# Optimization experiments

Measured on AMD Instinct MI355X. Metric: run time of the kernel, lower is better.

## Reference

```python
import jax, jax.numpy as jnp
import numpy as np

N = 50000
E = 800000
H = 8          # attention heads
C = 16         # per-head channels (128 // 8)
D = 128        # in_channels == num_hidden_channels
L = 2          # num_layers
NEG_SLOPE = 0.2
LN_EPS = 1e-12


def setup_inputs() -> dict:
    key = jax.random.key(0)
    ks = jax.random.split(key, 8)
    x = jax.random.normal(ks[0], (N, D), dtype=jnp.float32)
    edge_index = jax.random.randint(ks[1], (2, E), 0, N).astype(jnp.int64)
    W = jax.random.normal(ks[2], (L, D, D), dtype=jnp.float32) * 0.1
    att = jax.random.normal(ks[3], (L, H, C), dtype=jnp.float32) * 0.1
    bias = jnp.zeros((L, D), dtype=jnp.float32)
    out_W = jax.random.normal(ks[4], (D, D), dtype=jnp.float32) * 0.1
    out_b = jnp.zeros((D,), dtype=jnp.float32)
    ln_g = jnp.ones((D,), dtype=jnp.float32)
    ln_b = jnp.zeros((D,), dtype=jnp.float32)
    return {"x": x, "edge_index": edge_index, "W": W, "att": att, "bias": bias,
            "out_W": out_W, "out_b": out_b, "ln_g": ln_g, "ln_b": ln_b,
            "num_trg_nodes": 25000}


def gatv2_conv(x, src, dst, W_l, a_l, b_l):
    # share_weights=True: same linear map for source and target nodes
    h = (x @ W_l).reshape(N, H, C)               # [N,H,C]
    hs = h[src]                                  # [E,H,C] gather source
    hd = h[dst]                                  # [E,H,C] gather target
    e = jax.nn.leaky_relu(hs + hd, NEG_SLOPE)    # GATv2: LeakyReLU before attention vector
    logits = jnp.einsum('ehc,hc->eh', e, a_l)    # [E,H]
    # segment softmax over edges grouped by destination node
    seg_max = jax.ops.segment_max(logits, dst, num_segments=N)   # [N,H]
    ex = jnp.exp(logits - seg_max[dst])
    seg_sum = jax.ops.segment_sum(ex, dst, num_segments=N)       # [N,H]
    alpha = ex / (seg_sum[dst] + 1e-16)                          # [E,H]
    msg = (hs * alpha[..., None]).reshape(E, H * C)              # weighted messages
    out = jax.ops.segment_sum(msg, dst, num_segments=N)          # [N,H*C]
    return out + b_l


def reference(x, edge_index, W, att, bias, out_W, out_b, ln_g, ln_b, num_trg_nodes):
    src = edge_index[0]
    dst = edge_index[1]
    for i in range(L):
        x = gatv2_conv(x, src, dst, W[i], att[i], bias[i])
        if i != L - 1:
            # eval mode: dropout is identity; torch nn.GELU is exact erf gelu
            x = jax.nn.gelu(x, approximate=False)
    # output head: Linear -> LayerNorm(eps=1e-12) -> Dropout(identity in eval)
    y = x[:num_trg_nodes] @ out_W + out_b
    mu = jnp.mean(y, axis=-1, keepdims=True)
    var = jnp.mean(jnp.square(y - mu), axis=-1, keepdims=True)
    y = (y - mu) / jnp.sqrt(var + LN_EPS) * ln_g + ln_b
    return y
```

## Files before the change

### kernel.cpp

```cpp
#include <hip/hip_runtime.h>
#include <math.h>


#define D 128
#define H 8
#define C 16
#define NBIN 256

typedef __attribute__((ext_vector_type(8))) short bf16x8v;
typedef __attribute__((ext_vector_type(4))) float f32x4v;

static __device__ __forceinline__ float bf2f(unsigned int u16) {
    union { unsigned int i; float f; } x; x.i = u16 << 16; return x.f;
}
static __device__ __forceinline__ unsigned short f2bf(float f) {
    union { float f; unsigned int i; } x; x.f = f;
    unsigned int r = x.i + 0x7fffu + ((x.i >> 16) & 1u);
    return (unsigned short)(r >> 16);
}
static __device__ __forceinline__ float gelu_f(float v) {
    return 0.5f * v * (1.0f + erff(v * 0.70710678118654752f));
}
static __device__ __forceinline__ float exp2_hw(float x) {
    float r;
    asm("v_exp_f32 %0, %1" : "=v"(r) : "v"(x));
    return r;
}
#define DPP_ADD(v, ctrl) \
    (v) += __builtin_bit_cast(float, __builtin_amdgcn_update_dpp( \
        0, __builtin_bit_cast(int, (v)), (ctrl), 0xf, 0xf, true))

template<int IN_BF, int OUT_BF, int GELU>
static __device__ __forceinline__ void gemm_body(
    int bid, const void* __restrict__ Xv, const unsigned short* __restrict__ Wt,
    const float* __restrict__ bias, void* __restrict__ Outv, int nrows)
{
    const int t  = threadIdx.x;
    const int l  = t & 63;
    const int wv = t >> 6;
    const int g  = l >> 4;
    const int r  = l & 15;
    const int m0 = bid * 64;
    const int row = m0 + wv * 16 + r;
    const bool rv = row < nrows;
    const uint4* Wt4 = reinterpret_cast<const uint4*>(Wt);

    bf16x8v afrag[4];
#pragma unroll
    for (int kk = 0; kk < 4; ++kk) {
        int kg = kk * 4 + g;
        float v[8];
        if (IN_BF) {
            uint4 q = make_uint4(0, 0, 0, 0);
            if (rv) q = reinterpret_cast<const uint4*>(Xv)[(size_t)row * 16 + kg];
            if (GELU) {
                unsigned int qq[4] = {q.x, q.y, q.z, q.w};
#pragma unroll
                for (int j = 0; j < 4; ++j) {
                    v[2 * j]     = gelu_f(bf2f(qq[j] & 0xffffu));
                    v[2 * j + 1] = gelu_f(bf2f(qq[j] >> 16));
                }
                short pk[8];
#pragma unroll
                for (int j = 0; j < 8; ++j) pk[j] = (short)f2bf(v[j]);
                afrag[kk] = *reinterpret_cast<bf16x8v*>(pk);
            } else {
                afrag[kk] = __builtin_bit_cast(bf16x8v, q);
            }
        } else {
            float4 a = make_float4(0.f, 0.f, 0.f, 0.f), b = a;
            if (rv) {
                a = reinterpret_cast<const float4*>(Xv)[(size_t)row * 32 + kg * 2];
                b = reinterpret_cast<const float4*>(Xv)[(size_t)row * 32 + kg * 2 + 1];
            }
            v[0] = a.x; v[1] = a.y; v[2] = a.z; v[3] = a.w;
            v[4] = b.x; v[5] = b.y; v[6] = b.z; v[7] = b.w;
            if (GELU) {
#pragma unroll
                for (int j = 0; j < 8; ++j) v[j] = gelu_f(v[j]);
            }
            short pk[8];
#pragma unroll
            for (int j = 0; j < 8; ++j) pk[j] = (short)f2bf(v[j]);
            afrag[kk] = *reinterpret_cast<bf16x8v*>(pk);
        }
    }

    f32x4v acc[8];
#pragma unroll
    for (int ct = 0; ct < 8; ++ct) acc[ct] = (f32x4v){0.f, 0.f, 0.f, 0.f};

    bf16x8v bA[8], bB[8];
#pragma unroll
    for (int ct = 0; ct < 8; ++ct)
        bA[ct] = __builtin_bit_cast(bf16x8v, Wt4[(ct * 16 + r) * 16 + g]);

#pragma unroll
    for (int kk = 0; kk < 4; ++kk) {
        if (kk < 3) {
            int kgn = (kk + 1) * 4 + g;
#pragma unroll
            for (int ct = 0; ct < 8; ++ct) {
                bf16x8v v = __builtin_bit_cast(bf16x8v, Wt4[(ct * 16 + r) * 16 + kgn]);
                if (kk & 1) bA[ct] = v; else bB[ct] = v;
            }
        }
#pragma unroll
        for (int ct = 0; ct < 8; ++ct) {
            bf16x8v b = (kk & 1) ? bB[ct] : bA[ct];
            acc[ct] = __builtin_amdgcn_mfma_f32_16x16x32_bf16(afrag[kk], b, acc[ct], 0, 0, 0);
        }
    }

#pragma unroll
    for (int ct = 0; ct < 8; ++ct) {
        int col = ct * 16 + r;
        float bj = bias ? bias[col] : 0.f;
#pragma unroll
        for (int i = 0; i < 4; ++i) {
            int rr = m0 + wv * 16 + g * 4 + i;
            if (rr < nrows) {
                float val = acc[ct][i] + bj;
                if (OUT_BF)
                    reinterpret_cast<unsigned short*>(Outv)[(size_t)rr * 128 + col] = f2bf(val);
                else
                    reinterpret_cast<float*>(Outv)[(size_t)rr * 128 + col] = val;
            }
        }
    }
}

__global__ __launch_bounds__(256) void gemm_head_ln(
    const void* __restrict__ Xv, const unsigned short* __restrict__ Wt,
    const float* __restrict__ outb, const float* __restrict__ lng,
    const float* __restrict__ lnb, float* __restrict__ Out, int nrows)
{
    const int t  = threadIdx.x;
    const int l  = t & 63;
    const int wv = t >> 6;
    const int g  = l >> 4;
    const int r  = l & 15;
    const int m0 = blockIdx.x * 64;
    const int row = m0 + wv * 16 + r;
    const bool rv = row < nrows;
    const uint4* Wt4 = reinterpret_cast<const uint4*>(Wt);

    bf16x8v afrag[4];
#pragma unroll
    for (int kk = 0; kk < 4; ++kk) {
        int kg = kk * 4 + g;
        uint4 q = make_uint4(0, 0, 0, 0);
        if (rv) q = reinterpret_cast<const uint4*>(Xv)[(size_t)row * 16 + kg];
        afrag[kk] = __builtin_bit_cast(bf16x8v, q);
    }

    f32x4v acc[8];
#pragma unroll
    for (int ct = 0; ct < 8; ++ct) acc[ct] = (f32x4v){0.f, 0.f, 0.f, 0.f};

#pragma unroll
    for (int kk = 0; kk < 4; ++kk) {
        int kg = kk * 4 + g;
#pragma unroll
        for (int ct = 0; ct < 8; ++ct) {
            bf16x8v b = __builtin_bit_cast(bf16x8v, Wt4[(ct * 16 + r) * 16 + kg]);
            acc[ct] = __builtin_amdgcn_mfma_f32_16x16x32_bf16(afrag[kk], b, acc[ct], 0, 0, 0);
        }
    }

    float gmm[8], bbb[8];
#pragma unroll
    for (int ct = 0; ct < 8; ++ct) {
        gmm[ct] = lng[ct * 16 + r];
        bbb[ct] = lnb[ct * 16 + r];
    }

#pragma unroll
    for (int i = 0; i < 4; ++i) {
        int rr = m0 + wv * 16 + g * 4 + i;
        if (rr >= nrows) continue;
        float v[8];
        float s = 0.f;
#pragma unroll
        for (int ct = 0; ct < 8; ++ct) {
            v[ct] = acc[ct][i] + outb[ct * 16 + r];
            s += v[ct];
        }
        DPP_ADD(s, 0xB1); DPP_ADD(s, 0x4E); DPP_ADD(s, 0x141); DPP_ADD(s, 0x140);
        float mu = s * (1.f / 128.f);
        float q = 0.f;
#pragma unroll
        for (int ct = 0; ct < 8; ++ct) {
            float dd = v[ct] - mu;
            q += dd * dd;
        }
        DPP_ADD(q, 0xB1); DPP_ADD(q, 0x4E); DPP_ADD(q, 0x141); DPP_ADD(q, 0x140);
        float inv = rsqrtf(q * (1.f / 128.f) + 1e-12f);
#pragma unroll
        for (int ct = 0; ct < 8; ++ct)
            Out[(size_t)rr * 128 + ct * 16 + r] = (v[ct] - mu) * inv * gmm[ct] + bbb[ct];
    }
}

__global__ __launch_bounds__(256) void prep_kernel(
    const float* __restrict__ W, const float* __restrict__ outW,
    unsigned short* __restrict__ wbf,
    const int* __restrict__ dst, int* __restrict__ bh,
    int E, int chunk, int nblk)
{
    __shared__ char smem[128 * 17 * 2];
    int t = threadIdx.x;
    if (blockIdx.x < 24) {
        unsigned short (*tile)[17] = reinterpret_cast<unsigned short (*)[17]>(smem);
        int blk = blockIdx.x;
        int mat = blk >> 3, s = blk & 7;
        const float* src = (mat < 2) ? (W + (size_t)mat * D * D) : outW;
        unsigned short* dstp = wbf + (size_t)mat * D * D;
        int n0 = s * 16;
#pragma unroll
        for (int it = 0; it < 8; ++it) {
            int idx = it * 256 + t;
            int k = idx >> 4, n = idx & 15;
            tile[k][n] = f2bf(src[k * D + n0 + n]);
        }
        __syncthreads();
#pragma unroll
        for (int it = 0; it < 8; ++it) {
            int idx = it * 256 + t;
            int n = idx >> 7, k = idx & 127;
            dstp[(size_t)(n0 + n) * D + k] = tile[k][n];
        }
    } else {
        int* h = reinterpret_cast<int*>(smem);
        int b = blockIdx.x - 24;
        h[t] = 0;
        __syncthreads();
        int lo = b * chunk, hi = min(E, lo + chunk);
        for (int i = lo + t; i < hi; i += 256) atomicAdd(&h[dst[i] >> 8], 1);
        __syncthreads();
        bh[t * nblk + b] = h[t];
    }
}

__global__ __launch_bounds__(256) void scan_gemm0(
    int* __restrict__ bh, int* __restrict__ tot, int nblk,
    const float* __restrict__ x, const unsigned short* __restrict__ wbf,
    void* __restrict__ hbuf, int nrows)
{
    __shared__ int sh[256];
    int t = threadIdx.x;
    if (blockIdx.x < NBIN) {
        int bin = blockIdx.x;
        int v = (t < nblk) ? bh[bin * nblk + t] : 0;
        sh[t] = v;
        __syncthreads();
#pragma unroll
        for (int off = 1; off < 256; off <<= 1) {
            int xq = (t >= off) ? sh[t - off] : 0;
            __syncthreads();
            sh[t] += xq;
            __syncthreads();
        }
        if (t < nblk) bh[bin * nblk + t] = sh[t] - v;
        if (t == 255) tot[bin] = sh[255];
    } else {
        gemm_body<0, 1, 0>(blockIdx.x - NBIN, x, wbf, nullptr, hbuf, nrows);
    }
}

__global__ __launch_bounds__(256) void gemm_l1(
    const void* __restrict__ Xv, const unsigned short* __restrict__ Wt,
    void* __restrict__ Outv, int nrows)
{
    gemm_body<1, 1, 1>(blockIdx.x, Xv, Wt, nullptr, Outv, nrows);
}

__global__ __launch_bounds__(256) void scatter_bucket2(
    const int* __restrict__ dst, const int* __restrict__ src,
    const int* __restrict__ bh, const int* __restrict__ tot,
    int2* __restrict__ bout, int E, int chunk, int nblk)
{
    __shared__ int sh[NBIN];
    __shared__ int cur[NBIN];
    int t = threadIdx.x, b = blockIdx.x;
    int tv = tot[t];
    sh[t] = tv;
    __syncthreads();
#pragma unroll
    for (int off = 1; off < 256; off <<= 1) {
        int x = (t >= off) ? sh[t - off] : 0;
        __syncthreads();
        sh[t] += x;
        __syncthreads();
    }
    cur[t] = (sh[t] - tv) + bh[t * nblk + b];
    __syncthreads();
    int lo = b * chunk, hi = min(E, lo + chunk);
    for (int i = lo + t; i < hi; i += 256) {
        int d = dst[i];
        int p = atomicAdd(&cur[d >> 8], 1);
        bout[p] = make_int2(src[i], d);
    }
}

__global__ __launch_bounds__(256) void fill_fused(
    const int2* __restrict__ bout, const int* __restrict__ tot,
    int* __restrict__ rowptr, int* __restrict__ slist, int N, int E)
{
    __shared__ int sh[NBIN];
    __shared__ int cnt[NBIN];
    __shared__ int cur[NBIN];
    int b = blockIdx.x, t = threadIdx.x;

    int tv = tot[t];
    sh[t] = tv;
    __syncthreads();
#pragma unroll
    for (int off = 1; off < 256; off <<= 1) {
        int x = (t >= off) ? sh[t - off] : 0;
        __syncthreads();
        sh[t] += x;
        __syncthreads();
    }
    int hi = sh[b];
    int lo = hi - tot[b];

    cnt[t] = 0;
    __syncthreads();
    for (int i = lo + t; i < hi; i += 256) atomicAdd(&cnt[bout[i].y & 255], 1);
    __syncthreads();

    int cv = cnt[t];
    sh[t] = cv;
    __syncthreads();
#pragma unroll
    for (int off = 1; off < 256; off <<= 1) {
        int x = (t >= off) ? sh[t - off] : 0;
        __syncthreads();
        sh[t] += x;
        __syncthreads();
    }
    int start = lo + sh[t] - cv;
    int d0 = b * 256 + t;
    if (d0 < N) rowptr[d0] = start;
    if (b == (int)gridDim.x - 1 && t == 255) rowptr[N] = E;
    cur[t] = start;
    __syncthreads();

    for (int i = lo + t; i < hi; i += 256) {
        int2 e = bout[i];
        int p = atomicAdd(&cur[e.y & 255], 1);
        slist[p] = e.x;
    }
}

#define PROC(u, k) \
    float h##k##x = bf2f((u) & 0xffffu), h##k##y = bf2f((u) >> 16); \
    float a##k = h##k##x + hdx; a##k = fmaxf(a##k, 0.2f * a##k); \
    float b##k = h##k##y + hdy; b##k = fmaxf(b##k, 0.2f * b##k); \
    float p##k = a##k * aw.x + b##k * aw.y; \
    DPP_ADD(p##k, 0xB1); DPP_ADD(p##k, 0x4E); DPP_ADD(p##k, 0x141); \
    float e##k = exp2_hw(p##k);

#define QUAD_BODY(U0, U1, U2, U3) \
    { PROC(U0, 0) PROC(U1, 1) PROC(U2, 2) PROC(U3, 3) \
      ssum += (e0 + e1) + (e2 + e3); \
      accx = fmaf(e0, h0x, fmaf(e1, h1x, fmaf(e2, h2x, fmaf(e3, h3x, accx)))); \
      accy = fmaf(e0, h0y, fmaf(e1, h1y, fmaf(e2, h2y, fmaf(e3, h3y, accy)))); }

__global__ __launch_bounds__(256) void aggregate(
    const unsigned int* __restrict__ Hm,
    const int* __restrict__ rowptr, const int* __restrict__ slist,
    const float* __restrict__ att, const float* __restrict__ bias,
    unsigned int* __restrict__ Outv, int n)
{
    int wid  = threadIdx.x >> 6;
    int lane = threadIdx.x & 63;
    int d = blockIdx.x * 4 + wid;
    if (d >= n) return;

    int beg = __builtin_amdgcn_readfirstlane(rowptr[d]);
    int end = __builtin_amdgcn_readfirstlane(rowptr[d + 1]);

    unsigned int ud = Hm[((unsigned)d << 6) | lane];
    float hdx = bf2f(ud & 0xffffu), hdy = bf2f(ud >> 16);
    float2 aw = reinterpret_cast<const float2*>(att)[lane];
    aw.x *= 1.44269504088896f;
    aw.y *= 1.44269504088896f;

    float ssum = 0.f, accx = 0.f, accy = 0.f;

    int nfull = (end - beg) >> 2;
    int ii = beg;
    unsigned cu0, cu1, cu2, cu3;
    if (nfull) {
        cu0 = Hm[((unsigned)slist[ii]     << 6) | lane];
        cu1 = Hm[((unsigned)slist[ii + 1] << 6) | lane];
        cu2 = Hm[((unsigned)slist[ii + 2] << 6) | lane];
        cu3 = Hm[((unsigned)slist[ii + 3] << 6) | lane];
    }
    for (int q = 1; q < nfull; ++q) {
        int j = ii + 4;
        unsigned nu0 = Hm[((unsigned)slist[j]     << 6) | lane];
        unsigned nu1 = Hm[((unsigned)slist[j + 1] << 6) | lane];
        unsigned nu2 = Hm[((unsigned)slist[j + 2] << 6) | lane];
        unsigned nu3 = Hm[((unsigned)slist[j + 3] << 6) | lane];
        QUAD_BODY(cu0, cu1, cu2, cu3)
        cu0 = nu0; cu1 = nu1; cu2 = nu2; cu3 = nu3;
        ii = j;
    }
    if (nfull) {
        QUAD_BODY(cu0, cu1, cu2, cu3)
        ii += 4;
    }
    for (; ii < end; ++ii) {
        unsigned u0 = Hm[((unsigned)slist[ii] << 6) | lane];
        PROC(u0, 9)
        ssum += e9;
        accx = fmaf(e9, h9x, accx);
        accy = fmaf(e9, h9y, accy);
    }

    float inv = 1.f / (ssum + 1e-16f);
    float2 bv = reinterpret_cast<const float2*>(bias)[lane];
    float ox = accx * inv + bv.x;
    float oy = accy * inv + bv.y;
    Outv[((unsigned)d << 6) | lane] =
        (unsigned int)f2bf(ox) | ((unsigned int)f2bf(oy) << 16);
}

extern "C" void kernel_launch(void* const* d_in, const int* in_sizes, int n_in,
                              void* d_out, int out_size, void* d_ws, size_t ws_size,
                              hipStream_t stream)
{
    const float* x    = (const float*)d_in[0];
    const int*   edge = (const int*)d_in[1];
    const float* W    = (const float*)d_in[2];
    const float* att  = (const float*)d_in[3];
    const float* bias = (const float*)d_in[4];
    const float* outW = (const float*)d_in[5];
    const float* outb = (const float*)d_in[6];
    const float* lng  = (const float*)d_in[7];
    const float* lnb  = (const float*)d_in[8];

    const int N  = in_sizes[0] / D;
    const int E  = in_sizes[1] / 2;
    const int NT = out_size / D;

    const int* srcp = edge;
    const int* dstp = edge + E;

    auto align256 = [](size_t v) { return (v + 255) & ~(size_t)255; };
    auto cdiv = [](int a, int b) { return (a + b - 1) / b; };

    const int CHUNK = cdiv(E, 256);
    const int NBLK  = cdiv(E, CHUNK);
    const int NBKT  = cdiv(N, 256);
    const int NG    = cdiv(N, 64);

    char* wp = (char*)d_ws;
    size_t off = 0;
    void* hbuf   = (void*)(wp + off); off += align256((size_t)N * D * 2);
    void* xbuf   = (void*)(wp + off); off += align256((size_t)N * D * 2);
    unsigned short* wbf = (unsigned short*)(wp + off); off += align256((size_t)3 * D * D * 2);
    int*  rowptr = (int*)(wp + off);  off += align256((size_t)(N + 1) * 4);
    int*  slist  = (int*)(wp + off);  off += align256((size_t)E * 4);
    int2* bout   = (int2*)(wp + off); off += align256((size_t)E * 8);
    int*  bh     = (int*)(wp + off);  off += align256((size_t)NBIN * NBLK * 4);
    int*  tot    = (int*)(wp + off);  off += align256((size_t)NBIN * 4);
    (void)n_in; (void)ws_size;

    prep_kernel<<<24 + NBLK, 256, 0, stream>>>(W, outW, wbf, dstp, bh, E, CHUNK, NBLK);
    scan_gemm0<<<NBIN + NG, 256, 0, stream>>>(bh, tot, NBLK, x, wbf, hbuf, N);
    scatter_bucket2<<<NBLK, 256, 0, stream>>>(dstp, srcp, bh, tot, bout, E, CHUNK, NBLK);
    fill_fused<<<NBKT, 256, 0, stream>>>(bout, tot, rowptr, slist, N, E);
    aggregate<<<cdiv(N, 4), 256, 0, stream>>>((unsigned int*)hbuf, rowptr, slist,
                                              att, bias, (unsigned int*)xbuf, N);
    gemm_l1<<<NG, 256, 0, stream>>>(xbuf, wbf + D * D, hbuf, N);
    aggregate<<<cdiv(N, 4), 256, 0, stream>>>((unsigned int*)hbuf, rowptr, slist,
                                              att + H * C, bias + D, (unsigned int*)xbuf, N);
    gemm_head_ln<<<cdiv(NT, 64), 256, 0, stream>>>(xbuf, wbf + 2 * D * D, outb,
                                                   lng, lnb, (float*)d_out, NT);
}
```

Measured before the change: 162.7 us.

## Co-schedule layer-0 GEMM with edge scatter; rewrite LeakyReLU via abs identity

The bin prefix scan now runs as its own small kernel, and the layer-0 GEMM is launched in the same grid as the edge bucket scatter rather than alongside the scan. This lets the GEMM overlap the heavier scatter stage, and the scan and GEMM are no longer tied to one shared launch. Separately, the per-edge LeakyReLU plus attention dot is rewritten as 0.6*v + 0.4*|v|, with the constants folded into two pre-scaled attention vectors. That turns max/mul into fma/abs chains in the hot aggregate loop, with a small floating-point rounding difference.

```diff
diff --git a/kernel.cpp b/kernel.cpp
--- a/kernel.cpp
+++ b/kernel.cpp
@@ -242,17 +242,39 @@
     }
 }
 
-__global__ __launch_bounds__(256) void scan_gemm0(
-    int* __restrict__ bh, int* __restrict__ tot, int nblk,
+__global__ __launch_bounds__(256) void bin_scan(
+    int* __restrict__ bh, int* __restrict__ tot, int nblk)
+{
+    __shared__ int sh[256];
+    int bin = blockIdx.x, t = threadIdx.x;
+    int v = (t < nblk) ? bh[bin * nblk + t] : 0;
+    sh[t] = v;
+    __syncthreads();
+#pragma unroll
+    for (int off = 1; off < 256; off <<= 1) {
+        int x = (t >= off) ? sh[t - off] : 0;
+        __syncthreads();
+        sh[t] += x;
+        __syncthreads();
+    }
+    if (t < nblk) bh[bin * nblk + t] = sh[t] - v;
+    if (t == 255) tot[bin] = sh[255];
+}
+
+__global__ __launch_bounds__(256) void scatter_gemm0(
+    const int* __restrict__ dst, const int* __restrict__ src,
+    const int* __restrict__ bh, const int* __restrict__ tot,
+    int2* __restrict__ bout, int E, int chunk, int nblk,
     const float* __restrict__ x, const unsigned short* __restrict__ wbf,
     void* __restrict__ hbuf, int nrows)
 {
-    __shared__ int sh[256];
+    __shared__ int sh[NBIN];
+    __shared__ int cur[NBIN];
     int t = threadIdx.x;
-    if (blockIdx.x < NBIN) {
-        int bin = blockIdx.x;
-        int v = (t < nblk) ? bh[bin * nblk + t] : 0;
-        sh[t] = v;
+    if (blockIdx.x < nblk) {
+        int b = blockIdx.x;
+        int tv = tot[t];
+        sh[t] = tv;
         __syncthreads();
 #pragma unroll
         for (int off = 1; off < 256; off <<= 1) {
@@ -261,10 +283,16 @@
             sh[t] += xq;
             __syncthreads();
         }
-        if (t < nblk) bh[bin * nblk + t] = sh[t] - v;
-        if (t == 255) tot[bin] = sh[255];
+        cur[t] = (sh[t] - tv) + bh[t * nblk + b];
+        __syncthreads();
+        int lo = b * chunk, hi = min(E, lo + chunk);
+        for (int i = lo + t; i < hi; i += 256) {
+            int d = dst[i];
+            int p = atomicAdd(&cur[d >> 8], 1);
+            bout[p] = make_int2(src[i], d);
+        }
     } else {
-        gemm_body<0, 1, 0>(blockIdx.x - NBIN, x, wbf, nullptr, hbuf, nrows);
+        gemm_body<0, 1, 0>(blockIdx.x - nblk, x, wbf, nullptr, hbuf, nrows);
     }
 }
 
@@ -273,34 +301,6 @@
     void* __restrict__ Outv, int nrows)
 {
     gemm_body<1, 1, 1>(blockIdx.x, Xv, Wt, nullptr, Outv, nrows);
-}
-
-__global__ __launch_bounds__(256) void scatter_bucket2(
-    const int* __restrict__ dst, const int* __restrict__ src,
-    const int* __restrict__ bh, const int* __restrict__ tot,
-    int2* __restrict__ bout, int E, int chunk, int nblk)
-{
-    __shared__ int sh[NBIN];
-    __shared__ int cur[NBIN];
-    int t = threadIdx.x, b = blockIdx.x;
-    int tv = tot[t];
-    sh[t] = tv;
-    __syncthreads();
-#pragma unroll
-    for (int off = 1; off < 256; off <<= 1) {
-        int x = (t >= off) ? sh[t - off] : 0;
-        __syncthreads();
-        sh[t] += x;
-        __syncthreads();
-    }
-    cur[t] = (sh[t] - tv) + bh[t * nblk + b];
-    __syncthreads();
-    int lo = b * chunk, hi = min(E, lo + chunk);
-    for (int i = lo + t; i < hi; i += 256) {
-        int d = dst[i];
-        int p = atomicAdd(&cur[d >> 8], 1);
-        bout[p] = make_int2(src[i], d);
-    }
 }
 
 __global__ __launch_bounds__(256) void fill_fused(
@@ -356,9 +356,9 @@
 
 #define PROC(u, k) \
     float h##k##x = bf2f((u) & 0xffffu), h##k##y = bf2f((u) >> 16); \
-    float a##k = h##k##x + hdx; a##k = fmaxf(a##k, 0.2f * a##k); \
-    float b##k = h##k##y + hdy; b##k = fmaxf(b##k, 0.2f * b##k); \
-    float p##k = a##k * aw.x + b##k * aw.y; \
+    float v##k##0 = h##k##x + hdx, v##k##1 = h##k##y + hdy; \
+    float p##k = fmaf(aw1.x, v##k##0, fmaf(aw2.x, fabsf(v##k##0), \
+                 fmaf(aw1.y, v##k##1, aw2.y * fabsf(v##k##1)))); \
     DPP_ADD(p##k, 0xB1); DPP_ADD(p##k, 0x4E); DPP_ADD(p##k, 0x141); \
     float e##k = exp2_hw(p##k);
 
@@ -385,8 +385,11 @@
     unsigned int ud = Hm[((unsigned)d << 6) | lane];
     float hdx = bf2f(ud & 0xffffu), hdy = bf2f(ud >> 16);
     float2 aw = reinterpret_cast<const float2*>(att)[lane];
-    aw.x *= 1.44269504088896f;
-    aw.y *= 1.44269504088896f;
+    float2 aw1, aw2;
+    aw1.x = aw.x * 0.86561702453f;
+    aw1.y = aw.y * 0.86561702453f;
+    aw2.x = aw.x * 0.57707801636f;
+    aw2.y = aw.y * 0.57707801636f;
 
     float ssum = 0.f, accx = 0.f, accy = 0.f;
 
@@ -471,8 +474,9 @@
     (void)n_in; (void)ws_size;
 
     prep_kernel<<<24 + NBLK, 256, 0, stream>>>(W, outW, wbf, dstp, bh, E, CHUNK, NBLK);
-    scan_gemm0<<<NBIN + NG, 256, 0, stream>>>(bh, tot, NBLK, x, wbf, hbuf, N);
-    scatter_bucket2<<<NBLK, 256, 0, stream>>>(dstp, srcp, bh, tot, bout, E, CHUNK, NBLK);
+    bin_scan<<<NBIN, 256, 0, stream>>>(bh, tot, NBLK);
+    scatter_gemm0<<<NBLK + NG, 256, 0, stream>>>(dstp, srcp, bh, tot, bout,
+                                                 E, CHUNK, NBLK, x, wbf, hbuf, N);
     fill_fused<<<NBKT, 256, 0, stream>>>(bout, tot, rowptr, slist, N, E);
     aggregate<<<cdiv(N, 4), 256, 0, stream>>>((unsigned int*)hbuf, rowptr, slist,
                                               att, bias, (unsigned int*)xbuf, N);
```

After: 154.6 us. 5.0% less time.
